# Kernel tuning notes

Measured on AMD Instinct MI355X. Metric: run time of the kernel, lower is better.

Reference implementation:

```python
import jax, jax.numpy as jnp
import numpy as np

S_MAX = 512   # BERT max positions (module filters spans to <=512)


def setup_inputs() -> dict:
    key = jax.random.key(0)
    k1, k2, k3, k4, k5 = jax.random.split(key, 5)
    B, S, H = 8, 512, 768
    E, M, C = 16, 4, 96
    embedding = jax.random.normal(k1, (B, S, H), dtype=jnp.float32)
    # mean-over-heads last-layer attention rows (row-stochastic-ish positives)
    attention = jax.random.uniform(k2, (B, S, S), dtype=jnp.float32)
    attention = attention / attention.sum(-1, keepdims=True)
    mention_starts = jax.random.randint(k3, (B, E, M), 0, 500, dtype=jnp.int32)
    mention_lengths = jax.random.randint(k4, (B, E, M), 1, 6, dtype=jnp.int32)
    labels = jax.random.randint(k5, (B, E, E, C), 0, 2, dtype=jnp.int32)
    return {"embedding": embedding, "attention": attention,
            "mention_starts": mention_starts, "mention_lengths": mention_lengths,
            "labels": labels}


def reference(embedding, attention, mention_starts, mention_lengths, labels):
    # embedding: [B,S,H] BERT last_hidden_state
    # attention: [B,S,S] last-layer attention averaged over heads
    # mention spans (start, end): tokens start+1 .. end inclusive (per original slicing)
    B, S, H = embedding.shape
    E = mention_starts.shape[1]
    s_idx = jnp.arange(S, dtype=jnp.int32)
    ends = mention_starts + mention_lengths
    # token membership mask per entity: union over its mentions. [B,E,S]
    mask = ((s_idx >= (mention_starts + 1)[..., None]) &
            (s_idx <= ends[..., None])).any(axis=2)
    maskf = mask.astype(embedding.dtype)
    count = jnp.maximum(maskf.sum(-1, keepdims=True), 1.0)  # [B,E,1]
    # context[e] = mean over selected tokens t of attention[t] @ embedding
    att_rows = jnp.einsum('bes,bst->bet', maskf, attention)          # summed attention rows
    context = jnp.einsum('bet,bth->beh', att_rows, embedding) / count  # [B,E,H]
    # doc[e] = logsumexp over selected token embeddings (per hidden dim)
    masked = jnp.where(mask[..., None], embedding[:, None, :, :], -jnp.inf)  # [B,E,S,H]
    doc = jax.scipy.special.logsumexp(masked, axis=2)                # [B,E,H]
    cls = embedding[:, 0]                                            # [B,H]
    # all ordered entity pairs h != t (use_negative=True path)
    hh, tt = np.nonzero(~np.eye(E, dtype=bool))                      # static, P = E*(E-1)
    P = hh.shape[0]
    feat = jnp.stack([
        jnp.broadcast_to(cls[:, None, :], (B, P, H)),
        doc[:, hh],
        doc[:, tt],
        context[:, hh] * context[:, tt],
    ], axis=2)                                                       # [B,P,4,H]
    feature_set = feat.reshape(B * P, 4, H)
    labels_out = labels[:, hh, tt].reshape(B * P, -1)                # [B*P,C]
    return feature_set, labels_out
```

## Files before the change

kernel.cpp:

```cpp
#include <hip/hip_runtime.h>
#include <math.h>

#define Bc 8
#define Sc 512
#define Hc 768
#define Ec 16
#define Mc 4
#define Cc 96
#define Pc 240


__global__ __launch_bounds__(256) void k_mask_att_doc(
    const float* __restrict__ emb, const float* __restrict__ att,
    const int* __restrict__ starts, const int* __restrict__ lens,
    float* __restrict__ att_rows, float* __restrict__ cnt,
    float* __restrict__ docv)
{
  int be = blockIdx.x;
  int b  = be >> 4;
  int tid = threadIdx.x;

  __shared__ int slist[32];
  __shared__ int n_sh;
  if (tid == 0) n_sh = 0;
  __syncthreads();

  int base = be * Mc;
  int st0 = starts[base+0], st1 = starts[base+1];
  int st2 = starts[base+2], st3 = starts[base+3];
  int en0 = st0 + lens[base+0], en1 = st1 + lens[base+1];
  int en2 = st2 + lens[base+2], en3 = st3 + lens[base+3];

  for (int s = tid; s < Sc; s += 256) {
    bool in = (s > st0 && s <= en0) || (s > st1 && s <= en1) ||
              (s > st2 && s <= en2) || (s > st3 && s <= en3);
    if (in) { int pos = atomicAdd(&n_sh, 1); slist[pos] = s; }
  }
  __syncthreads();
  int n = n_sh;

  float a0 = 0.f, a1 = 0.f;
  for (int i = 0; i < n; ++i) {
    const float* row = att + ((size_t)b * Sc + slist[i]) * Sc;
    a0 += row[tid];
    a1 += row[tid + 256];
  }
  float* arow = att_rows + (size_t)be * Sc;
  arow[tid]       = a0;
  arow[tid + 256] = a1;
  if (tid == 0) cnt[be] = (float)n;

  #pragma unroll
  for (int kk = 0; kk < 3; ++kk) {
    int h = tid + kk * 256;
    const float* ecol = emb + (size_t)b * Sc * Hc + h;
    float m = ecol[(size_t)slist[0] * Hc];
    float l = 1.0f;
    for (int i = 1; i < n; ++i) {
      float v  = ecol[(size_t)slist[i] * Hc];
      float nm = fmaxf(m, v);
      l = l * __expf(m - nm) + __expf(v - nm);
      m = nm;
    }
    docv[(size_t)be * Hc + h] = m + __logf(l);
  }
}

__global__ __launch_bounds__(256) void k_context(
    const float* __restrict__ emb, const float* __restrict__ att_rows,
    float* __restrict__ ctxu)
{
  int tchunk = blockIdx.x;
  int hchunk = blockIdx.y;
  int b      = blockIdx.z;
  int tid = threadIdx.x;
  int h  = hchunk * 256 + tid;
  int t0 = tchunk * 128;

  __shared__ float ar[128][16];
  for (int idx = tid; idx < 128 * 16; idx += 256) {
    int e = idx & 15, tt = idx >> 4;
    ar[tt][e] = att_rows[((size_t)(b * Ec + e)) * Sc + t0 + tt];
  }
  __syncthreads();

  float acc[16];
  #pragma unroll
  for (int e = 0; e < 16; ++e) acc[e] = 0.f;

  const float* ecol = emb + ((size_t)b * Sc + t0) * Hc + h;
  for (int tt = 0; tt < 128; ++tt) {
    float ev = ecol[(size_t)tt * Hc];
    #pragma unroll
    for (int e = 0; e < 16; ++e) acc[e] = fmaf(ar[tt][e], ev, acc[e]);
  }

  float* outb = ctxu + (size_t)(b * Ec) * Hc + h;
  #pragma unroll
  for (int e = 0; e < 16; ++e) atomicAdd(outb + (size_t)e * Hc, acc[e]);
}

__global__ __launch_bounds__(256) void k_assemble(
    const float* __restrict__ emb, const int* __restrict__ labels,
    const float* __restrict__ docv, const float* __restrict__ ctxu,
    const float* __restrict__ cnt, float* __restrict__ out)
{
  int r = blockIdx.x;
  int b = r / Pc, p = r % Pc;
  int i = p / 15, k = p % 15;
  int j = k + (k >= i ? 1 : 0);
  int tid = threadIdx.x;

  float ci = 1.0f / cnt[b * Ec + i];
  float cj = 1.0f / cnt[b * Ec + j];

  size_t rowbase = (size_t)r * 4 * Hc;
  const float* clsrow = emb  + (size_t)b * Sc * Hc;
  const float* di_ = docv + (size_t)(b * Ec + i) * Hc;
  const float* dj_ = docv + (size_t)(b * Ec + j) * Hc;
  const float* xi_ = ctxu + (size_t)(b * Ec + i) * Hc;
  const float* xj_ = ctxu + (size_t)(b * Ec + j) * Hc;

  #pragma unroll
  for (int kk = 0; kk < 3; ++kk) {
    int h = tid + kk * 256;
    out[rowbase +           h] = clsrow[h];
    out[rowbase +     Hc  + h] = di_[h];
    out[rowbase + 2 * Hc  + h] = dj_[h];
    out[rowbase + 3 * Hc  + h] = (xi_[h] * ci) * (xj_[h] * cj);
  }

  if (tid < Cc) {
    const int* lrow = labels + (((size_t)b * Ec + i) * Ec + j) * Cc;
    out[(size_t)Bc * Pc * 4 * Hc + (size_t)r * Cc + tid] = (float)lrow[tid];
  }
}

extern "C" void kernel_launch(void* const* d_in, const int* in_sizes, int n_in,
                              void* d_out, int out_size, void* d_ws, size_t ws_size,
                              hipStream_t stream) {
  const float* emb    = (const float*)d_in[0];
  const float* att    = (const float*)d_in[1];
  const int*   starts = (const int*)d_in[2];
  const int*   lens   = (const int*)d_in[3];
  const int*   labels = (const int*)d_in[4];
  float* out = (float*)d_out;

  float* att_rows = (float*)d_ws;
  float* cnt      = att_rows + (size_t)Bc * Ec * Sc;
  float* docv     = cnt      + (size_t)Bc * Ec;
  float* ctxu     = docv     + (size_t)Bc * Ec * Hc;

  hipMemsetAsync(ctxu, 0, (size_t)Bc * Ec * Hc * sizeof(float), stream);

  k_mask_att_doc<<<Bc * Ec, 256, 0, stream>>>(emb, att, starts, lens,
                                              att_rows, cnt, docv);
  k_context<<<dim3(4, 3, Bc), 256, 0, stream>>>(emb, att_rows, ctxu);
  k_assemble<<<Bc * Pc, 256, 0, stream>>>(emb, labels, docv, ctxu, cnt, out);
}
```

Before: 105.4 us.

## Vectorize loads/stores, fold memset into first kernel, split context over more blocks

Replaces the separate memset of the context accumulator by zeroing it inside the first kernel. It vectorizes the attention row sums (float2), the assemble kernel (float4 with 192 threads) and the label conversion (int4). The context kernel now splits T into 64-token chunks across twice as many blocks, reading the padded shared tile with float4. This cuts launch overhead and memory instructions and raises parallelism in the context step, at the cost of twice as many atomic adds.

```diff
diff --git a/kernel.cpp b/kernel.cpp
--- a/kernel.cpp
+++ b/kernel.cpp
@@ -14,11 +14,16 @@
     const float* __restrict__ emb, const float* __restrict__ att,
     const int* __restrict__ starts, const int* __restrict__ lens,
     float* __restrict__ att_rows, float* __restrict__ cnt,
-    float* __restrict__ docv)
+    float* __restrict__ docv, float* __restrict__ ctxu)
 {
   int be = blockIdx.x;
   int b  = be >> 4;
   int tid = threadIdx.x;
+
+  {
+    float* z = ctxu + (size_t)be * Hc;
+    z[tid] = 0.f; z[tid + 256] = 0.f; z[tid + 512] = 0.f;
+  }
 
   __shared__ int slist[32];
   __shared__ int n_sh;
@@ -39,15 +44,14 @@
   __syncthreads();
   int n = n_sh;
 
-  float a0 = 0.f, a1 = 0.f;
+  float2 a = make_float2(0.f, 0.f);
   for (int i = 0; i < n; ++i) {
-    const float* row = att + ((size_t)b * Sc + slist[i]) * Sc;
-    a0 += row[tid];
-    a1 += row[tid + 256];
+    const float2* row2 =
+        (const float2*)(att + ((size_t)b * Sc + slist[i]) * Sc);
+    float2 v = row2[tid];
+    a.x += v.x; a.y += v.y;
   }
-  float* arow = att_rows + (size_t)be * Sc;
-  arow[tid]       = a0;
-  arow[tid + 256] = a1;
+  ((float2*)(att_rows + (size_t)be * Sc))[tid] = a;
   if (tid == 0) cnt[be] = (float)n;
 
   #pragma unroll
@@ -75,12 +79,18 @@
   int b      = blockIdx.z;
   int tid = threadIdx.x;
   int h  = hchunk * 256 + tid;
-  int t0 = tchunk * 128;
+  int t0 = tchunk * 64;
 
-  __shared__ float ar[128][16];
-  for (int idx = tid; idx < 128 * 16; idx += 256) {
-    int e = idx & 15, tt = idx >> 4;
-    ar[tt][e] = att_rows[((size_t)(b * Ec + e)) * Sc + t0 + tt];
+  __shared__ float ar[64][20];
+  {
+    int e = tid >> 4, q = tid & 15;
+    const float4* src =
+        (const float4*)(att_rows + ((size_t)(b * Ec + e)) * Sc + t0);
+    float4 v = src[q];
+    ar[q*4+0][e] = v.x;
+    ar[q*4+1][e] = v.y;
+    ar[q*4+2][e] = v.z;
+    ar[q*4+3][e] = v.w;
   }
   __syncthreads();
 
@@ -89,10 +99,27 @@
   for (int e = 0; e < 16; ++e) acc[e] = 0.f;
 
   const float* ecol = emb + ((size_t)b * Sc + t0) * Hc + h;
-  for (int tt = 0; tt < 128; ++tt) {
+  #pragma unroll 4
+  for (int tt = 0; tt < 64; ++tt) {
     float ev = ecol[(size_t)tt * Hc];
-    #pragma unroll
-    for (int e = 0; e < 16; ++e) acc[e] = fmaf(ar[tt][e], ev, acc[e]);
+    const float4* arv = (const float4*)&ar[tt][0];
+    float4 a0 = arv[0], a1 = arv[1], a2 = arv[2], a3 = arv[3];
+    acc[ 0] = fmaf(a0.x, ev, acc[ 0]);
+    acc[ 1] = fmaf(a0.y, ev, acc[ 1]);
+    acc[ 2] = fmaf(a0.z, ev, acc[ 2]);
+    acc[ 3] = fmaf(a0.w, ev, acc[ 3]);
+    acc[ 4] = fmaf(a1.x, ev, acc[ 4]);
+    acc[ 5] = fmaf(a1.y, ev, acc[ 5]);
+    acc[ 6] = fmaf(a1.z, ev, acc[ 6]);
+    acc[ 7] = fmaf(a1.w, ev, acc[ 7]);
+    acc[ 8] = fmaf(a2.x, ev, acc[ 8]);
+    acc[ 9] = fmaf(a2.y, ev, acc[ 9]);
+    acc[10] = fmaf(a2.z, ev, acc[10]);
+    acc[11] = fmaf(a2.w, ev, acc[11]);
+    acc[12] = fmaf(a3.x, ev, acc[12]);
+    acc[13] = fmaf(a3.y, ev, acc[13]);
+    acc[14] = fmaf(a3.z, ev, acc[14]);
+    acc[15] = fmaf(a3.w, ev, acc[15]);
   }
 
   float* outb = ctxu + (size_t)(b * Ec) * Hc + h;
@@ -100,7 +127,7 @@
   for (int e = 0; e < 16; ++e) atomicAdd(outb + (size_t)e * Hc, acc[e]);
 }
 
-__global__ __launch_bounds__(256) void k_assemble(
+__global__ __launch_bounds__(192) void k_assemble(
     const float* __restrict__ emb, const int* __restrict__ labels,
     const float* __restrict__ docv, const float* __restrict__ ctxu,
     const float* __restrict__ cnt, float* __restrict__ out)
@@ -114,25 +141,30 @@
   float ci = 1.0f / cnt[b * Ec + i];
   float cj = 1.0f / cnt[b * Ec + j];
 
-  size_t rowbase = (size_t)r * 4 * Hc;
-  const float* clsrow = emb  + (size_t)b * Sc * Hc;
-  const float* di_ = docv + (size_t)(b * Ec + i) * Hc;
-  const float* dj_ = docv + (size_t)(b * Ec + j) * Hc;
-  const float* xi_ = ctxu + (size_t)(b * Ec + i) * Hc;
-  const float* xj_ = ctxu + (size_t)(b * Ec + j) * Hc;
+  const float4* cls4 = (const float4*)(emb  + (size_t)b * Sc * Hc);
+  const float4* di4  = (const float4*)(docv + (size_t)(b * Ec + i) * Hc);
+  const float4* dj4  = (const float4*)(docv + (size_t)(b * Ec + j) * Hc);
+  const float4* xi4  = (const float4*)(ctxu + (size_t)(b * Ec + i) * Hc);
+  const float4* xj4  = (const float4*)(ctxu + (size_t)(b * Ec + j) * Hc);
+  float4* o = (float4*)(out + (size_t)r * 4 * Hc);
 
-  #pragma unroll
-  for (int kk = 0; kk < 3; ++kk) {
-    int h = tid + kk * 256;
-    out[rowbase +           h] = clsrow[h];
-    out[rowbase +     Hc  + h] = di_[h];
-    out[rowbase + 2 * Hc  + h] = dj_[h];
-    out[rowbase + 3 * Hc  + h] = (xi_[h] * ci) * (xj_[h] * cj);
-  }
+  o[      tid] = cls4[tid];
+  o[192 + tid] = di4[tid];
+  o[384 + tid] = dj4[tid];
+  float4 xa = xi4[tid], xb = xj4[tid], c;
+  c.x = (xa.x * ci) * (xb.x * cj);
+  c.y = (xa.y * ci) * (xb.y * cj);
+  c.z = (xa.z * ci) * (xb.z * cj);
+  c.w = (xa.w * ci) * (xb.w * cj);
+  o[576 + tid] = c;
 
-  if (tid < Cc) {
-    const int* lrow = labels + (((size_t)b * Ec + i) * Ec + j) * Cc;
-    out[(size_t)Bc * Pc * 4 * Hc + (size_t)r * Cc + tid] = (float)lrow[tid];
+  if (tid < 24) {
+    const int4* l4 =
+        (const int4*)(labels + (((size_t)b * Ec + i) * Ec + j) * Cc);
+    int4 v = l4[tid];
+    float4 f;
+    f.x = (float)v.x; f.y = (float)v.y; f.z = (float)v.z; f.w = (float)v.w;
+    ((float4*)(out + (size_t)Bc * Pc * 4 * Hc + (size_t)r * Cc))[tid] = f;
   }
 }
 
@@ -151,10 +183,8 @@
   float* docv     = cnt      + (size_t)Bc * Ec;
   float* ctxu     = docv     + (size_t)Bc * Ec * Hc;
 
-  hipMemsetAsync(ctxu, 0, (size_t)Bc * Ec * Hc * sizeof(float), stream);
-
   k_mask_att_doc<<<Bc * Ec, 256, 0, stream>>>(emb, att, starts, lens,
-                                              att_rows, cnt, docv);
-  k_context<<<dim3(4, 3, Bc), 256, 0, stream>>>(emb, att_rows, ctxu);
-  k_assemble<<<Bc * Pc, 256, 0, stream>>>(emb, labels, docv, ctxu, cnt, out);
+                                              att_rows, cnt, docv, ctxu);
+  k_context<<<dim3(8, 3, Bc), 256, 0, stream>>>(emb, att_rows, ctxu);
+  k_assemble<<<Bc * Pc, 192, 0, stream>>>(emb, labels, docv, ctxu, cnt, out);
 }
```

After: 98.86 us. -6.2%, faster.
